# Performance work log

Hardware: AMD Instinct MI355X
Metric: run time of the kernel (lower is better)

## Reference

```python
import jax, jax.numpy as jnp
import numpy as np
import math

HIDDEN = 1024
NUM_HEADS = 16
HEAD_DIM = HIDDEN // NUM_HEADS
B, S = 4, 1024


def setup_inputs() -> dict:
    key = jax.random.key(0)
    ks = jax.random.split(key, 16)
    sd = 1.0 / math.sqrt(HIDDEN)
    inp = {
        "x": jax.random.normal(ks[0], (B, S, HIDDEN), jnp.float32),
        "spikes": jax.random.uniform(ks[1], (B, S, HIDDEN), jnp.float32),
        "membrane_potential": jax.random.normal(ks[2], (B, S, HIDDEN), jnp.float32),
        "Wq": jax.random.normal(ks[3], (HIDDEN, HIDDEN), jnp.float32) * sd,
        "bq": jnp.zeros((HIDDEN,), jnp.float32),
        "Wk": jax.random.normal(ks[4], (HIDDEN, HIDDEN), jnp.float32) * sd,
        "bk": jnp.zeros((HIDDEN,), jnp.float32),
        "Wv": jax.random.normal(ks[5], (HIDDEN, HIDDEN), jnp.float32) * sd,
        "bv": jnp.zeros((HIDDEN,), jnp.float32),
        "Wo": jax.random.normal(ks[6], (HIDDEN, HIDDEN), jnp.float32) * sd,
        "bo": jnp.zeros((HIDDEN,), jnp.float32),
        "tau_decay": jnp.ones((NUM_HEADS,), jnp.float32) * 10.0,
        "Wg": jax.random.normal(ks[7], (HIDDEN, 2 * HIDDEN), jnp.float32) * sd,
        "bg": jnp.zeros((HIDDEN,), jnp.float32),
    }
    return inp


def _heads(t):  # [B,S,H] -> [B,nH,S,hd]
    Bv, Sv, _ = t.shape
    return t.reshape(Bv, Sv, NUM_HEADS, HEAD_DIM).transpose(0, 2, 1, 3)


def reference(x, spikes, membrane_potential, Wq, bq, Wk, bk, Wv, bv, Wo, bo, tau_decay, Wg, bg):
    scale = 1.0 / math.sqrt(HEAD_DIM)
    q = _heads(x @ Wq.T + bq)
    k = _heads(x @ Wk.T + bk)
    v = _heads(x @ Wv.T + bv)

    # raw scores [B,nH,S,S]
    scores = jnp.einsum('bhqd,bhkd->bhqk', q, k) * scale

    # per-head exponential temporal decay mask [nH,S,S]
    times = jnp.arange(S, dtype=jnp.float32)
    tdiff = jnp.abs(times[:, None] - times[None, :])  # [S,S]
    tmask = jnp.exp(-tdiff[None] / tau_decay[:, None, None])
    scores = scores * tmask[None]

    # spike correlation term
    sm = _heads(spikes)
    spike_attn = jnp.einsum('bhqd,bhkd->bhqk', sm, sm) * scale
    scores = scores * (1.0 + spike_attn)

    # membrane gating of V
    v = v * jax.nn.sigmoid(_heads(membrane_potential))

    probs = jax.nn.softmax(scores, axis=-1)
    context = jnp.einsum('bhqk,bhkd->bhqd', probs, v)
    context = context.transpose(0, 2, 1, 3).reshape(B, S, HIDDEN)

    # dendritic gate
    gate_in = jnp.concatenate([context, membrane_potential], axis=-1)
    gate = jax.nn.sigmoid(gate_in @ Wg.T + bg)
    context = context * gate

    return context @ Wo.T + bo
```

## Files before the change

### kernel.cpp

```cpp
#include <hip/hip_runtime.h>
#include <math.h>
#include <stdint.h>

namespace {

typedef __attribute__((ext_vector_type(8))) short s8v;
typedef __attribute__((ext_vector_type(4))) float f4v;
typedef unsigned short u16;

__device__ __forceinline__ float fexp2(float x) {
  return __builtin_amdgcn_exp2f(x);
}

__device__ __forceinline__ u16 f2bf(float f) {
  union { float f; uint32_t u; } v; v.f = f;
  uint32_t r = v.u + 0x7fffu + ((v.u >> 16) & 1u);
  return (u16)(r >> 16);
}
__device__ __forceinline__ float bf2f(u16 h) {
  union { uint32_t u; float f; } v; v.u = ((uint32_t)h) << 16;
  return v.f;
}
__device__ __forceinline__ uint32_t pk2r(float a, float b) {
  return (uint32_t)f2bf(a) | ((uint32_t)f2bf(b) << 16);
}
__device__ __forceinline__ uint32_t pk2(float a, float b) {
  union { float f; uint32_t u; } x, y; x.f = a; y.f = b;
  return ((x.u + 0x8000u) >> 16) | ((y.u + 0x8000u) & 0xffff0000u);
}
__device__ __forceinline__ float sigmoidf_(float x) { return 1.0f / (1.0f + __expf(-x)); }

__device__ __forceinline__ void gload16(const u16* g, u16* l) {
  __builtin_amdgcn_global_load_lds(
      (const __attribute__((address_space(1))) void*)g,
      (__attribute__((address_space(3))) void*)l, 16, 0, 0);
}

struct CvtJob { const float* src; u16* dst; };
struct CvtArgs { CvtJob j[14]; };

__global__ __launch_bounds__(256) void cvt_kernel(CvtArgs a) {
  const CvtJob jb = a.j[blockIdx.y];
  const int i = blockIdx.x * 256 + threadIdx.x;
  const float4 v = ((const float4*)jb.src)[i];
  uint2 pk;
  pk.x = pk2r(v.x, v.y);
  pk.y = pk2r(v.z, v.w);
  ((uint2*)jb.dst)[i] = pk;
}

__global__ __launch_bounds__(256) void qkv_gemm(
    const u16* __restrict__ xb,
    const u16* __restrict__ Wqb, const u16* __restrict__ Wkb, const u16* __restrict__ Wvb,
    const float* __restrict__ bq, const float* __restrict__ bk, const float* __restrict__ bv,
    const float* __restrict__ mem,
    u16* __restrict__ Qb, u16* __restrict__ Kb, u16* __restrict__ Vt) {
  __shared__ u16 as_[8192], bs_[8192];
  const int t = threadIdx.x;
  const int nb = blockIdx.x, mb = blockIdx.y;
  const int sel = nb >> 3;
  const u16* W = sel == 0 ? Wqb : (sel == 1 ? Wkb : Wvb);
  const float* bias = sel == 0 ? bq : (sel == 1 ? bk : bv);
  const int m0 = mb * 128, n0 = (nb & 7) * 128;
  const f4v fz = {0.f, 0.f, 0.f, 0.f};
  f4v acc[4][4];
#pragma unroll
  for (int i = 0; i < 4; ++i)
#pragma unroll
    for (int j = 0; j < 4; ++j) acc[i][j] = fz;

  const int l = t & 63, w = t >> 6, wm = w >> 1, wn = w & 1;
  const int lr = l & 15, lq = l >> 4;
  const int rx = lr & 7;
  const int srow = t >> 3;
  const int scol = ((t & 7) ^ (srow & 7)) * 8;

#define QKV_STAGE(k0)                                                          \
  {                                                                            \
    const int kk_ = (k0);                                                      \
    _Pragma("unroll") for (int u = 0; u < 4; ++u) {                            \
      gload16(xb + (size_t)(m0 + u * 32 + srow) * 1024 + kk_ + scol,           \
              as_ + u * 2048 + t * 8);                                         \
      gload16(W + (size_t)(n0 + u * 32 + srow) * 1024 + kk_ + scol,            \
              bs_ + u * 2048 + t * 8);                                         \
    }                                                                          \
  }

  QKV_STAGE(0);

  if (sel < 2) {
    for (int c = 0; c < 16; ++c) {
      __syncthreads();
      s8v af[2][4], bf[2][4];
#pragma unroll
      for (int ks = 0; ks < 2; ++ks) {
        const int co = ((ks * 4 + lq) ^ rx) * 8;
#pragma unroll
        for (int mi = 0; mi < 4; ++mi)
          af[ks][mi] = *(const s8v*)(as_ + (wm * 64 + mi * 16 + lr) * 64 + co);
#pragma unroll
        for (int ni = 0; ni < 4; ++ni)
          bf[ks][ni] = *(const s8v*)(bs_ + (wn * 64 + ni * 16 + lr) * 64 + co);
      }
      __syncthreads();
      if (c < 15) QKV_STAGE((c + 1) << 6);
#pragma unroll
      for (int ks = 0; ks < 2; ++ks)
#pragma unroll
        for (int mi = 0; mi < 4; ++mi)
#pragma unroll
          for (int ni = 0; ni < 4; ++ni)
            acc[mi][ni] = __builtin_amdgcn_mfma_f32_16x16x32_bf16(
                bf[ks][ni], af[ks][mi], acc[mi][ni], 0, 0, 0);
    }
    u16* dst = (sel == 0) ? Qb : Kb;
#pragma unroll
    for (int mi = 0; mi < 4; ++mi)
#pragma unroll
      for (int ni = 0; ni < 4; ++ni) {
        const int m = m0 + wm * 64 + mi * 16 + lr;
        const int nb4 = n0 + wn * 64 + ni * 16 + lq * 4;
        const float4 b4 = *(const float4*)&bias[nb4];
        uint2 pk;
        pk.x = pk2r(acc[mi][ni][0] + b4.x, acc[mi][ni][1] + b4.y);
        pk.y = pk2r(acc[mi][ni][2] + b4.z, acc[mi][ni][3] + b4.w);
        *(uint2*)(dst + (size_t)m * 1024 + nb4) = pk;
      }
  } else {
    for (int c = 0; c < 16; ++c) {
      __syncthreads();
      s8v af[2][4], bf[2][4];
#pragma unroll
      for (int ks = 0; ks < 2; ++ks) {
        const int co = ((ks * 4 + lq) ^ rx) * 8;
#pragma unroll
        for (int mi = 0; mi < 4; ++mi)
          af[ks][mi] = *(const s8v*)(as_ + (wm * 64 + mi * 16 + lr) * 64 + co);
#pragma unroll
        for (int ni = 0; ni < 4; ++ni)
          bf[ks][ni] = *(const s8v*)(bs_ + (wn * 64 + ni * 16 + lr) * 64 + co);
      }
      __syncthreads();
      if (c < 15) QKV_STAGE((c + 1) << 6);
#pragma unroll
      for (int ks = 0; ks < 2; ++ks)
#pragma unroll
        for (int mi = 0; mi < 4; ++mi)
#pragma unroll
          for (int ni = 0; ni < 4; ++ni)
            acc[mi][ni] = __builtin_amdgcn_mfma_f32_16x16x32_bf16(
                af[ks][mi], bf[ks][ni], acc[mi][ni], 0, 0, 0);
    }
    const int b = m0 >> 10;
#pragma unroll
    for (int mi = 0; mi < 4; ++mi)
#pragma unroll
      for (int ni = 0; ni < 4; ++ni) {
        const int mrow = m0 + wm * 64 + mi * 16 + lq * 4;
        const int ncol = n0 + wn * 64 + ni * 16 + lr;
        const int h = ncol >> 6, d = ncol & 63;
        const float bi = bias[ncol];
        float tv[4];
#pragma unroll
        for (int r = 0; r < 4; ++r)
          tv[r] = (acc[mi][ni][r] + bi) * sigmoidf_(mem[(size_t)(mrow + r) * 1024 + ncol]);
        const int s = mrow & 1023;
        uint2 pk;
        pk.x = pk2r(tv[0], tv[1]);
        pk.y = pk2r(tv[2], tv[3]);
        *(uint2*)(Vt + ((size_t)((b * 16 + h) * 64 + d)) * 1024 + s) = pk;
      }
  }
#undef QKV_STAGE
}

template <int MODE>
__global__ __launch_bounds__(256) void gemm64(
    const u16* __restrict__ Ab, const u16* __restrict__ A2b,
    const u16* __restrict__ W, const float* __restrict__ bias,
    u16* __restrict__ outb, float* __restrict__ outf, int K) {
  __shared__ u16 as_[4096], bs_[8192];
  const int t = threadIdx.x, l = t & 63, w = t >> 6;
  const int wm = w >> 1, wn = w & 1, lr = l & 15, lq = l >> 4;
  const int m0 = blockIdx.y * 64, n0 = blockIdx.x * 128;
  const f4v fz = {0.f, 0.f, 0.f, 0.f};
  f4v acc[2][4];
#pragma unroll
  for (int i = 0; i < 2; ++i)
#pragma unroll
    for (int j = 0; j < 4; ++j) acc[i][j] = fz;
  const int rx = lr & 7;
  const int srow = t >> 3;
  const int scol = ((t & 7) ^ (srow & 7)) * 8;
  const int nc = K >> 6;

#define G64_STAGE(k0)                                                          \
  {                                                                            \
    const int kk_ = (k0);                                                      \
    const u16* Ae_ = Ab;                                                       \
    int ka_ = kk_;                                                             \
    if (MODE == 1 && kk_ >= 1024) { Ae_ = A2b; ka_ = kk_ - 1024; }             \
    _Pragma("unroll") for (int u = 0; u < 2; ++u)                              \
        gload16(Ae_ + (size_t)(m0 + u * 32 + srow) * 1024 + ka_ + scol,        \
                as_ + u * 2048 + t * 8);                                       \
    _Pragma("unroll") for (int u = 0; u < 4; ++u)                              \
        gload16(W + (size_t)(n0 + u * 32 + srow) * K + kk_ + scol,             \
                bs_ + u * 2048 + t * 8);                                       \
  }

  G64_STAGE(0);
  for (int c = 0; c < nc; ++c) {
    __syncthreads();
    s8v af[2][2], bf[2][4];
#pragma unroll
    for (int ks = 0; ks < 2; ++ks) {
      const int co = ((ks * 4 + lq) ^ rx) * 8;
#pragma unroll
      for (int mi = 0; mi < 2; ++mi)
        af[ks][mi] = *(const s8v*)(as_ + (wm * 32 + mi * 16 + lr) * 64 + co);
#pragma unroll
      for (int ni = 0; ni < 4; ++ni)
        bf[ks][ni] = *(const s8v*)(bs_ + (wn * 64 + ni * 16 + lr) * 64 + co);
    }
    __syncthreads();
    if (c + 1 < nc) G64_STAGE((c + 1) << 6);
#pragma unroll
    for (int ks = 0; ks < 2; ++ks)
#pragma unroll
      for (int mi = 0; mi < 2; ++mi)
#pragma unroll
        for (int ni = 0; ni < 4; ++ni)
          acc[mi][ni] = __builtin_amdgcn_mfma_f32_16x16x32_bf16(
              bf[ks][ni], af[ks][mi], acc[mi][ni], 0, 0, 0);
  }
#undef G64_STAGE

#pragma unroll
  for (int mi = 0; mi < 2; ++mi)
#pragma unroll
    for (int ni = 0; ni < 4; ++ni) {
      const int m = m0 + wm * 32 + mi * 16 + lr;
      const int nb4 = n0 + wn * 64 + ni * 16 + lq * 4;
      const float4 b4 = *(const float4*)&bias[nb4];
      if (MODE == 0) {
        float4 o;
        o.x = acc[mi][ni][0] + b4.x; o.y = acc[mi][ni][1] + b4.y;
        o.z = acc[mi][ni][2] + b4.z; o.w = acc[mi][ni][3] + b4.w;
        *(float4*)(outf + (size_t)m * 1024 + nb4) = o;
      } else {
        const uint2 a2 = *(const uint2*)(Ab + (size_t)m * 1024 + nb4);
        float cx[4] = {bf2f((u16)(a2.x & 0xffff)), bf2f((u16)(a2.x >> 16)),
                       bf2f((u16)(a2.y & 0xffff)), bf2f((u16)(a2.y >> 16))};
        float g[4];
        g[0] = cx[0] * sigmoidf_(acc[mi][ni][0] + b4.x);
        g[1] = cx[1] * sigmoidf_(acc[mi][ni][1] + b4.y);
        g[2] = cx[2] * sigmoidf_(acc[mi][ni][2] + b4.z);
        g[3] = cx[3] * sigmoidf_(acc[mi][ni][3] + b4.w);
        uint2 pk;
        pk.x = pk2r(g[0], g[1]);
        pk.y = pk2r(g[2], g[3]);
        *(uint2*)(outb + (size_t)m * 1024 + nb4) = pk;
      }
    }
}

__global__ __launch_bounds__(256) void attn_mfma(
    const u16* __restrict__ Qb, const u16* __restrict__ Kb,
    const u16* __restrict__ SPb, const u16* __restrict__ Vt,
    const float* __restrict__ tau, u16* __restrict__ CTXb) {
  __shared__ u16 kbuf[4096], skbuf[4096], vbuf[4096];
  __shared__ u16 pbuf[4][16 * 64];
  const int t = threadIdx.x, l = t & 63, w = t >> 6;
  const int lr = l & 15, lq = l >> 4;
  const int p = blockIdx.x;
  const int g = (p & 7) + 8 * (p >> 7);
  const int qt = (p >> 3) & 15;
  const int h = g & 15, b = g >> 4;

  const float c2 = 1.44269504088896f / tau[h];
  const float K0 = 0.125f * 1.44269504088896f;
  float cN[4], cNi[4], cR[4], cRi[4];
#pragma unroll
  for (int i = 0; i < 4; ++i) {
    cN[i]  = fexp2(c2 * (float)(i * 16));
    cNi[i] = fexp2(-c2 * (float)(i * 16));
    cR[i]  = fexp2(c2 * (float)(lq * 4 + i));
    cRi[i] = fexp2(-c2 * (float)(lq * 4 + i));
  }

  s8v qf[2], sf[2];
  {
    const size_t base = ((size_t)(b * 1024 + qt * 64 + w * 16 + lr)) * 1024 + h * 64 + lq * 8;
    qf[0] = *(const s8v*)(Qb + base);
    qf[1] = *(const s8v*)(Qb + base + 32);
    sf[0] = *(const s8v*)(SPb + base);
    sf[1] = *(const s8v*)(SPb + base + 32);
  }

  const f4v fz = {0.f, 0.f, 0.f, 0.f};
  f4v oacc[4];
  float lacc[4];
#pragma unroll
  for (int i = 0; i < 4; ++i) { oacc[i] = fz; lacc[i] = 0.f; }

  const int iqw = qt * 64 + w * 16;
  const int srow = t >> 3;
  const int csw = ((t & 7) ^ (srow & 7)) * 8;
  const int rx = lr & 7;
  u16* pw = pbuf[w];

  for (int jc = 0; jc < 16; ++jc) {
    const int j0 = jc * 64;
    __syncthreads();
    {
      const size_t kg = ((size_t)(b * 1024 + j0 + srow)) * 1024 + h * 64 + csw;
      gload16(Kb + kg, kbuf + t * 8);
      gload16(Kb + kg + 32 * 1024, kbuf + 2048 + t * 8);
      gload16(SPb + kg, skbuf + t * 8);
      gload16(SPb + kg + 32 * 1024, skbuf + 2048 + t * 8);
      const size_t vg = ((size_t)((b * 16 + h) * 64 + srow)) * 1024 + j0 + csw;
      gload16(Vt + vg, vbuf + t * 8);
      gload16(Vt + vg + 32 * 1024, vbuf + 2048 + t * 8);
    }
    __syncthreads();

    f4v sa[4], ssa[4];
#pragma unroll
    for (int ni = 0; ni < 4; ++ni) { sa[ni] = fz; ssa[ni] = fz; }
#pragma unroll
    for (int ks = 0; ks < 2; ++ks) {
#pragma unroll
      for (int ni = 0; ni < 4; ++ni) {
        const int off = (ni * 16 + lr) * 64 + (((ks * 4 + lq) ^ rx) * 8);
        const s8v kf = *(const s8v*)(kbuf + off);
        sa[ni] = __builtin_amdgcn_mfma_f32_16x16x32_bf16(kf, qf[ks], sa[ni], 0, 0, 0);
        const s8v skf = *(const s8v*)(skbuf + off);
        ssa[ni] = __builtin_amdgcn_mfma_f32_16x16x32_bf16(skf, sf[ks], ssa[ni], 0, 0, 0);
      }
    }

    const int D0 = iqw - j0;
    float pv[4][4];
    if (jc < qt) {
      const float EA = K0 * fexp2(-c2 * (float)(D0 + lr));
#pragma unroll
      for (int ni = 0; ni < 4; ++ni)
#pragma unroll
        for (int r = 0; r < 4; ++r) {
          const float t1 = fmaf(ssa[ni][r], 0.125f, 1.0f);
          const float sc2 = sa[ni][r] * cN[ni] * cR[r] * EA * t1;
          const float e = fexp2(sc2);
          pv[ni][r] = e;
          lacc[ni] += e;
        }
    } else if (jc > qt) {
      const float EAi = K0 * fexp2(c2 * (float)(D0 + lr));
#pragma unroll
      for (int ni = 0; ni < 4; ++ni)
#pragma unroll
        for (int r = 0; r < 4; ++r) {
          const float t1 = fmaf(ssa[ni][r], 0.125f, 1.0f);
          const float sc2 = sa[ni][r] * cNi[ni] * cRi[r] * EAi * t1;
          const float e = fexp2(sc2);
          pv[ni][r] = e;
          lacc[ni] += e;
        }
    } else {
      const float EA  = K0 * fexp2(-c2 * (float)(D0 + lr));
      const float EAi = K0 * fexp2(c2 * (float)(D0 + lr));
#pragma unroll
      for (int ni = 0; ni < 4; ++ni)
#pragma unroll
        for (int r = 0; r < 4; ++r) {
          const int jloc = ni * 16 + lq * 4 + r;
          const float fb = cN[ni] * cR[r] * EA;
          const float fa = cNi[ni] * cRi[r] * EAi;
          const float f = (D0 + lr >= jloc) ? fb : fa;
          const float t1 = fmaf(ssa[ni][r], 0.125f, 1.0f);
          const float e = fexp2(sa[ni][r] * f * t1);
          pv[ni][r] = e;
          lacc[ni] += e;
        }
    }

#pragma unroll
    for (int ni = 0; ni < 4; ++ni) {
      const int phys = (ni * 2 + (lq >> 1)) ^ rx;
      uint2 p2;
      p2.x = pk2(pv[ni][0], pv[ni][1]);
      p2.y = pk2(pv[ni][2], pv[ni][3]);
      *(uint2*)(pw + lr * 64 + phys * 8 + (lq & 1) * 4) = p2;
    }

#pragma unroll
    for (int ks = 0; ks < 2; ++ks) {
      const s8v pf = *(const s8v*)(pw + lr * 64 + (((ks * 4 + lq) ^ rx) * 8));
#pragma unroll
      for (int nd = 0; nd < 4; ++nd) {
        const int off = (nd * 16 + lr) * 64 + (((ks * 4 + lq) ^ rx) * 8);
        const s8v vf = *(const s8v*)(vbuf + off);
        oacc[nd] = __builtin_amdgcn_mfma_f32_16x16x32_bf16(vf, pf, oacc[nd], 0, 0, 0);
      }
    }
  }

  float ls = (lacc[0] + lacc[1]) + (lacc[2] + lacc[3]);
  ls += __shfl_xor(ls, 16);
  ls += __shfl_xor(ls, 32);
  const float inv = 1.0f / ls;
  const size_t orow = ((size_t)(b * 1024 + qt * 64 + w * 16 + lr)) * 1024 + h * 64;
#pragma unroll
  for (int nd = 0; nd < 4; ++nd) {
    uint2 o;
    o.x = pk2r(oacc[nd][0] * inv, oacc[nd][1] * inv);
    o.y = pk2r(oacc[nd][2] * inv, oacc[nd][3] * inv);
    *(uint2*)(CTXb + orow + nd * 16 + lq * 4) = o;
  }
}

}

extern "C" void kernel_launch(void* const* d_in, const int* in_sizes, int n_in,
                              void* d_out, int out_size, void* d_ws, size_t ws_size,
                              hipStream_t stream) {
  const float* x      = (const float*)d_in[0];
  const float* spikes = (const float*)d_in[1];
  const float* mem    = (const float*)d_in[2];
  const float* Wq     = (const float*)d_in[3];
  const float* bq     = (const float*)d_in[4];
  const float* Wk     = (const float*)d_in[5];
  const float* bk     = (const float*)d_in[6];
  const float* Wv     = (const float*)d_in[7];
  const float* bv     = (const float*)d_in[8];
  const float* Wo     = (const float*)d_in[9];
  const float* bo     = (const float*)d_in[10];
  const float* tau    = (const float*)d_in[11];
  const float* Wg     = (const float*)d_in[12];
  const float* bg     = (const float*)d_in[13];
  float* out = (float*)d_out;

  uint8_t* w8 = (uint8_t*)d_ws;
  u16* spb  = (u16*)(w8);
  u16* xb   = (u16*)(w8 + (8u << 20));
  u16* Wqb  = (u16*)(w8 + (16u << 20));
  u16* Wkb  = (u16*)(w8 + (18u << 20));
  u16* Wvb  = (u16*)(w8 + (20u << 20));
  u16* Wob  = (u16*)(w8 + (22u << 20));
  u16* Wgb  = (u16*)(w8 + (24u << 20));
  u16* Qb   = (u16*)(w8 + (28u << 20));
  u16* Kb   = (u16*)(w8 + (36u << 20));
  u16* Vt   = (u16*)(w8 + (44u << 20));
  u16* CTXb = (u16*)(w8 + (52u << 20));
  u16* memb = Qb;
  u16* gctx = xb;

  constexpr size_t QE = 262144 * 4;
  CvtArgs ca;
  for (int q = 0; q < 4; ++q) ca.j[q]     = {x + q * QE,      xb + q * QE};
  for (int q = 0; q < 4; ++q) ca.j[4 + q] = {spikes + q * QE, spb + q * QE};
  ca.j[8]  = {Wq, Wqb};
  ca.j[9]  = {Wk, Wkb};
  ca.j[10] = {Wv, Wvb};
  ca.j[11] = {Wo, Wob};
  ca.j[12] = {Wg, Wgb};
  ca.j[13] = {Wg + QE, Wgb + QE};
  cvt_kernel<<<dim3(1024, 14), 256, 0, stream>>>(ca);

  qkv_gemm<<<dim3(24, 32), 256, 0, stream>>>(xb, Wqb, Wkb, Wvb, bq, bk, bv, mem,
                                             Qb, Kb, Vt);
  attn_mfma<<<dim3(1024), 256, 0, stream>>>(Qb, Kb, spb, Vt, tau, CTXb);

  CvtArgs cm;
  for (int q = 0; q < 4; ++q) cm.j[q] = {mem + q * QE, memb + q * QE};
  cvt_kernel<<<dim3(1024, 4), 256, 0, stream>>>(cm);

  gemm64<1><<<dim3(8, 64), 256, 0, stream>>>(CTXb, memb, Wgb, bg, gctx, nullptr, 2048);
  gemm64<0><<<dim3(8, 64), 256, 0, stream>>>(gctx, nullptr, Wob, bo, nullptr, out, 1024);
}
```

Baseline: 278.1 us.

## Double-buffer LDS in GEMMs and fold membrane conversion into first cvt launch

Both the QKV GEMM and the gate/output GEMMs now use ping-pong LDS buffers. The next K-tile's global-to-LDS load is issued right after one barrier and overlaps with the MFMA work on the current tile, which removes the second barrier per iteration. The membrane-potential bf16 conversion moves into the initial batched cvt launch, using the output buffer as scratch, so one kernel launch disappears. LDS use doubles, which may lower occupancy. The output buffer is also overwritten later, so this relies on the kernels running in order.

```diff
diff --git a/kernel.cpp b/kernel.cpp
--- a/kernel.cpp
+++ b/kernel.cpp
@@ -37,7 +37,7 @@
 }
 
 struct CvtJob { const float* src; u16* dst; };
-struct CvtArgs { CvtJob j[14]; };
+struct CvtArgs { CvtJob j[18]; };
 
 __global__ __launch_bounds__(256) void cvt_kernel(CvtArgs a) {
   const CvtJob jb = a.j[blockIdx.y];
@@ -55,7 +55,7 @@
     const float* __restrict__ bq, const float* __restrict__ bk, const float* __restrict__ bv,
     const float* __restrict__ mem,
     u16* __restrict__ Qb, u16* __restrict__ Kb, u16* __restrict__ Vt) {
-  __shared__ u16 as_[8192], bs_[8192];
+  __shared__ u16 as_[16384], bs_[16384];
   const int t = threadIdx.x;
   const int nb = blockIdx.x, mb = blockIdx.y;
   const int sel = nb >> 3;
@@ -75,43 +75,44 @@
   const int srow = t >> 3;
   const int scol = ((t & 7) ^ (srow & 7)) * 8;
 
-#define QKV_STAGE(k0)                                                          \
+#define QKV_STAGE(k0, bsel)                                                    \
   {                                                                            \
     const int kk_ = (k0);                                                      \
+    const int lo_ = (bsel) * 8192;                                             \
     _Pragma("unroll") for (int u = 0; u < 4; ++u) {                            \
       gload16(xb + (size_t)(m0 + u * 32 + srow) * 1024 + kk_ + scol,           \
-              as_ + u * 2048 + t * 8);                                         \
+              as_ + lo_ + u * 2048 + t * 8);                                   \
       gload16(W + (size_t)(n0 + u * 32 + srow) * 1024 + kk_ + scol,            \
-              bs_ + u * 2048 + t * 8);                                         \
+              bs_ + lo_ + u * 2048 + t * 8);                                   \
     }                                                                          \
   }
 
-  QKV_STAGE(0);
+  QKV_STAGE(0, 0);
+  int pp = 0;
 
   if (sel < 2) {
     for (int c = 0; c < 16; ++c) {
       __syncthreads();
-      s8v af[2][4], bf[2][4];
+      if (c < 15) QKV_STAGE((c + 1) << 6, pp ^ 1);
+      const int lo = pp * 8192;
 #pragma unroll
       for (int ks = 0; ks < 2; ++ks) {
         const int co = ((ks * 4 + lq) ^ rx) * 8;
+        s8v af[4], bf[4];
 #pragma unroll
         for (int mi = 0; mi < 4; ++mi)
-          af[ks][mi] = *(const s8v*)(as_ + (wm * 64 + mi * 16 + lr) * 64 + co);
+          af[mi] = *(const s8v*)(as_ + lo + (wm * 64 + mi * 16 + lr) * 64 + co);
 #pragma unroll
         for (int ni = 0; ni < 4; ++ni)
-          bf[ks][ni] = *(const s8v*)(bs_ + (wn * 64 + ni * 16 + lr) * 64 + co);
-      }
-      __syncthreads();
-      if (c < 15) QKV_STAGE((c + 1) << 6);
-#pragma unroll
-      for (int ks = 0; ks < 2; ++ks)
+          bf[ni] = *(const s8v*)(bs_ + lo + (wn * 64 + ni * 16 + lr) * 64 + co);
 #pragma unroll
         for (int mi = 0; mi < 4; ++mi)
 #pragma unroll
           for (int ni = 0; ni < 4; ++ni)
             acc[mi][ni] = __builtin_amdgcn_mfma_f32_16x16x32_bf16(
-                bf[ks][ni], af[ks][mi], acc[mi][ni], 0, 0, 0);
+                bf[ni], af[mi], acc[mi][ni], 0, 0, 0);
+      }
+      pp ^= 1;
     }
     u16* dst = (sel == 0) ? Qb : Kb;
 #pragma unroll
@@ -129,27 +130,26 @@
   } else {
     for (int c = 0; c < 16; ++c) {
       __syncthreads();
-      s8v af[2][4], bf[2][4];
+      if (c < 15) QKV_STAGE((c + 1) << 6, pp ^ 1);
+      const int lo = pp * 8192;
 #pragma unroll
       for (int ks = 0; ks < 2; ++ks) {
         const int co = ((ks * 4 + lq) ^ rx) * 8;
+        s8v af[4], bf[4];
 #pragma unroll
         for (int mi = 0; mi < 4; ++mi)
-          af[ks][mi] = *(const s8v*)(as_ + (wm * 64 + mi * 16 + lr) * 64 + co);
+          af[mi] = *(const s8v*)(as_ + lo + (wm * 64 + mi * 16 + lr) * 64 + co);
 #pragma unroll
         for (int ni = 0; ni < 4; ++ni)
-          bf[ks][ni] = *(const s8v*)(bs_ + (wn * 64 + ni * 16 + lr) * 64 + co);
-      }
-      __syncthreads();
-      if (c < 15) QKV_STAGE((c + 1) << 6);
-#pragma unroll
-      for (int ks = 0; ks < 2; ++ks)
+          bf[ni] = *(const s8v*)(bs_ + lo + (wn * 64 + ni * 16 + lr) * 64 + co);
 #pragma unroll
         for (int mi = 0; mi < 4; ++mi)
 #pragma unroll
           for (int ni = 0; ni < 4; ++ni)
             acc[mi][ni] = __builtin_amdgcn_mfma_f32_16x16x32_bf16(
-                af[ks][mi], bf[ks][ni], acc[mi][ni], 0, 0, 0);
+                af[mi], bf[ni], acc[mi][ni], 0, 0, 0);
+      }
+      pp ^= 1;
     }
     const int b = m0 >> 10;
 #pragma unroll
@@ -179,7 +179,7 @@
     const u16* __restrict__ Ab, const u16* __restrict__ A2b,
     const u16* __restrict__ W, const float* __restrict__ bias,
     u16* __restrict__ outb, float* __restrict__ outf, int K) {
-  __shared__ u16 as_[4096], bs_[8192];
+  __shared__ u16 as_[8192], bs_[16384];
   const int t = threadIdx.x, l = t & 63, w = t >> 6;
   const int wm = w >> 1, wn = w & 1, lr = l & 15, lq = l >> 4;
   const int m0 = blockIdx.y * 64, n0 = blockIdx.x * 128;
@@ -194,7 +194,7 @@
   const int scol = ((t & 7) ^ (srow & 7)) * 8;
   const int nc = K >> 6;
 
-#define G64_STAGE(k0)                                                          \
+#define G64_STAGE(k0, bsel)                                                    \
   {                                                                            \
     const int kk_ = (k0);                                                      \
     const u16* Ae_ = Ab;                                                       \
@@ -202,36 +202,36 @@
     if (MODE == 1 && kk_ >= 1024) { Ae_ = A2b; ka_ = kk_ - 1024; }             \
     _Pragma("unroll") for (int u = 0; u < 2; ++u)                              \
         gload16(Ae_ + (size_t)(m0 + u * 32 + srow) * 1024 + ka_ + scol,        \
-                as_ + u * 2048 + t * 8);                                       \
+                as_ + (bsel) * 4096 + u * 2048 + t * 8);                       \
     _Pragma("unroll") for (int u = 0; u < 4; ++u)                              \
         gload16(W + (size_t)(n0 + u * 32 + srow) * K + kk_ + scol,             \
-                bs_ + u * 2048 + t * 8);                                       \
-  }
-
-  G64_STAGE(0);
+                bs_ + (bsel) * 8192 + u * 2048 + t * 8);                       \
+  }
+
+  G64_STAGE(0, 0);
+  int pp = 0;
   for (int c = 0; c < nc; ++c) {
     __syncthreads();
-    s8v af[2][2], bf[2][4];
+    if (c + 1 < nc) G64_STAGE((c + 1) << 6, pp ^ 1);
+    const int loA = pp * 4096, loB = pp * 8192;
 #pragma unroll
     for (int ks = 0; ks < 2; ++ks) {
       const int co = ((ks * 4 + lq) ^ rx) * 8;
+      s8v af[2], bf[4];
 #pragma unroll
       for (int mi = 0; mi < 2; ++mi)
-        af[ks][mi] = *(const s8v*)(as_ + (wm * 32 + mi * 16 + lr) * 64 + co);
+        af[mi] = *(const s8v*)(as_ + loA + (wm * 32 + mi * 16 + lr) * 64 + co);
 #pragma unroll
       for (int ni = 0; ni < 4; ++ni)
-        bf[ks][ni] = *(const s8v*)(bs_ + (wn * 64 + ni * 16 + lr) * 64 + co);
-    }
-    __syncthreads();
-    if (c + 1 < nc) G64_STAGE((c + 1) << 6);
-#pragma unroll
-    for (int ks = 0; ks < 2; ++ks)
+        bf[ni] = *(const s8v*)(bs_ + loB + (wn * 64 + ni * 16 + lr) * 64 + co);
 #pragma unroll
       for (int mi = 0; mi < 2; ++mi)
 #pragma unroll
         for (int ni = 0; ni < 4; ++ni)
           acc[mi][ni] = __builtin_amdgcn_mfma_f32_16x16x32_bf16(
-              bf[ks][ni], af[ks][mi], acc[mi][ni], 0, 0, 0);
+              bf[ni], af[mi], acc[mi][ni], 0, 0, 0);
+    }
+    pp ^= 1;
   }
 #undef G64_STAGE
 
@@ -451,29 +451,25 @@
   u16* Kb   = (u16*)(w8 + (36u << 20));
   u16* Vt   = (u16*)(w8 + (44u << 20));
   u16* CTXb = (u16*)(w8 + (52u << 20));
-  u16* memb = Qb;
+  u16* memb = (u16*)d_out;
   u16* gctx = xb;
 
   constexpr size_t QE = 262144 * 4;
   CvtArgs ca;
   for (int q = 0; q < 4; ++q) ca.j[q]     = {x + q * QE,      xb + q * QE};
   for (int q = 0; q < 4; ++q) ca.j[4 + q] = {spikes + q * QE, spb + q * QE};
-  ca.j[8]  = {Wq, Wqb};
-  ca.j[9]  = {Wk, Wkb};
-  ca.j[10] = {Wv, Wvb};
-  ca.j[11] = {Wo, Wob};
-  ca.j[12] = {Wg, Wgb};
-  ca.j[13] = {Wg + QE, Wgb + QE};
-  cvt_kernel<<<dim3(1024, 14), 256, 0, stream>>>(ca);
+  for (int q = 0; q < 4; ++q) ca.j[8 + q] = {mem + q * QE,    memb + q * QE};
+  ca.j[12] = {Wq, Wqb};
+  ca.j[13] = {Wk, Wkb};
+  ca.j[14] = {Wv, Wvb};
+  ca.j[15] = {Wo, Wob};
+  ca.j[16] = {Wg, Wgb};
+  ca.j[17] = {Wg + QE, Wgb + QE};
+  cvt_kernel<<<dim3(1024, 18), 256, 0, stream>>>(ca);
 
   qkv_gemm<<<dim3(24, 32), 256, 0, stream>>>(xb, Wqb, Wkb, Wvb, bq, bk, bv, mem,
                                              Qb, Kb, Vt);
   attn_mfma<<<dim3(1024), 256, 0, stream>>>(Qb, Kb, spb, Vt, tau, CTXb);
-
-  CvtArgs cm;
-  for (int q = 0; q < 4; ++q) cm.j[q] = {mem + q * QE, memb + q * QE};
-  cvt_kernel<<<dim3(1024, 4), 256, 0, stream>>>(cm);
-
   gemm64<1><<<dim3(8, 64), 256, 0, stream>>>(CTXb, memb, Wgb, bg, gctx, nullptr, 2048);
   gemm64<0><<<dim3(8, 64), 256, 0, stream>>>(gctx, nullptr, Wob, bo, nullptr, out, 1024);
 }
```

Result: no change. 281.8 us (+1.3%).
